# Performance work log

Hardware: AMD Instinct MI355X
Metric: run time of the kernel (lower is better)

The kernel has to match this reference:

```python
import jax, jax.numpy as jnp
import numpy as np

B, S, D_MODEL, D_K, D_V = 4, 2048, 512, 64, 64
TEMPERATURE = 8.0  # sqrt(d_k)


def setup_inputs() -> dict:
    key = jax.random.key(0)
    ks = jax.random.split(key, 12)
    q = jax.random.normal(ks[0], (B, S, D_MODEL), jnp.float32)
    k = jax.random.normal(ks[1], (B, S, D_MODEL), jnp.float32)
    v = jax.random.normal(ks[2], (B, S, D_MODEL), jnp.float32)
    g_bias = jax.random.normal(ks[3], (B, S, S), jnp.float32)
    mask = jax.random.bernoulli(ks[4], 0.25, (B, S, S))  # True = masked out
    sq = np.sqrt(2.0 / (D_MODEL + D_K)).astype(np.float32)
    sv = np.sqrt(2.0 / (D_MODEL + D_V)).astype(np.float32)
    Wq = jax.random.normal(ks[5], (D_MODEL, D_K), jnp.float32) * sq
    Wk = jax.random.normal(ks[6], (D_MODEL, D_K), jnp.float32) * sq
    Wv = jax.random.normal(ks[7], (D_MODEL, D_V), jnp.float32) * sv
    bq = jnp.zeros((D_K,), jnp.float32)
    bk = jnp.zeros((D_K,), jnp.float32)
    bv = jnp.zeros((D_V,), jnp.float32)
    lim = np.sqrt(6.0 / (D_V + D_MODEL)).astype(np.float32)  # xavier_uniform
    Wfc = jax.random.uniform(ks[8], (D_V, D_MODEL), jnp.float32, -lim, lim)
    bfc = jnp.zeros((D_MODEL,), jnp.float32)
    tau = jnp.float32(30.0)
    return {"q": q, "k": k, "v": v, "g_bias": g_bias, "mask": mask,
            "Wq": Wq, "bq": bq, "Wk": Wk, "bk": bk, "Wv": Wv, "bv": bv,
            "Wfc": Wfc, "bfc": bfc, "tau": tau}


def reference(q, k, v, g_bias, mask, Wq, bq, Wk, bk, Wv, bv, Wfc, bfc, tau):
    qp = q @ Wq + bq                                   # [B,S,dk]
    kp = k @ Wk + bk                                   # [B,S,dk]
    vp = v @ Wv + bv                                   # [B,S,dv]
    attn = jnp.einsum('bqd,bkd->bqk', qp, kp) / TEMPERATURE
    attn = attn + g_bias / (2.0 * tau ** 2)            # temperature-dependent Gaussian bias
    attn = jnp.where(mask, -jnp.inf, attn)
    p = jax.nn.softmax(attn, axis=2)                   # dropout = identity (eval mode)
    out = jnp.einsum('bqk,bkd->bqd', p, vp)            # [B,S,dv]
    return out @ Wfc + bfc                             # [B,S,d_model]
```

## Files before the change

### kernel.cpp

```cpp
#include <hip/hip_runtime.h>

#define NB 4
#define SS 2048
#define DM 512
#define DD 64
#define NR (NB*SS)
#define PH 128
#define NKS 8

typedef __attribute__((ext_vector_type(8))) short bf16x8;
typedef __attribute__((ext_vector_type(4))) float f32x4;

static __device__ __forceinline__ unsigned short f2b(float f) {
  union { float f; unsigned u; } x; x.f = f;
  unsigned r = x.u + 0x7FFFu + ((x.u >> 16) & 1u);
  return (unsigned short)(r >> 16);
}
static __device__ __forceinline__ float b2f(unsigned short h) {
  union { unsigned u; float f; } x; x.u = ((unsigned)h) << 16; return x.f;
}
static __device__ __forceinline__ bf16x8 ld8(const unsigned short* p) {
  union { uint4 u; bf16x8 v; } x; x.u = *(const uint4*)p; return x.v;
}
static __device__ __forceinline__ void glds16(const void* g, void* l) {
  auto gp = (const __attribute__((address_space(1))) unsigned*)((__UINTPTR_TYPE__)g);
  auto lp = (__attribute__((address_space(3))) unsigned*)((__UINTPTR_TYPE__)l);
  __builtin_amdgcn_global_load_lds(gp, lp, 16, 0, 0);
}

__global__ __launch_bounds__(256) void detect_mask(const unsigned* __restrict__ mw,
                                                   int nwords, int* __restrict__ part) {
  const int gid = blockIdx.x * 256 + threadIdx.x;
  const int nthr = gridDim.x * 256;
  int vi = 0, vf = 0, vu = 0;
  for (long i = (long)gid * 64; i < nwords; i += (long)nthr * 64) {
    unsigned w = mw[i];
    vi |= (w > 1u);
    vf |= ((w != 0u) & (w != 0x3F800000u));
    vu |= ((w & 0xFEFEFEFEu) != 0u);
  }
  __shared__ int sh[3];
  if (threadIdx.x < 3) sh[threadIdx.x] = 0;
  __syncthreads();
  int lane = threadIdx.x & 63;
  unsigned long long b;
  b = __ballot(vi); if (lane == 0 && b) sh[0] = 1;
  b = __ballot(vf); if (lane == 0 && b) sh[1] = 1;
  b = __ballot(vu); if (lane == 0 && b) sh[2] = 1;
  __syncthreads();
  if (threadIdx.x < 3) part[blockIdx.x * 4 + threadIdx.x] = sh[threadIdx.x];
}

__global__ __launch_bounds__(256) void prep(
    const float* __restrict__ Wq, const float* __restrict__ Wk, const float* __restrict__ Wv,
    unsigned short* __restrict__ Wt,
    const float* __restrict__ Wfc, unsigned short* __restrict__ WfcT) {
  const int bid = blockIdx.x;
  const int t = threadIdx.x;
  if (bid < 24) {
    const int p = bid >> 3;
    const float* W = (p == 0) ? Wq : ((p == 1) ? Wk : Wv);
    const int k0 = (bid & 7) * 64;
    const int n0 = (t & 15) * 4;
    #pragma unroll
    for (int p2 = 0; p2 < 4; ++p2) {
      int k = k0 + (t >> 4) + 16 * p2;
      float4 w = *(const float4*)(W + (size_t)k * DD + n0);
      Wt[(size_t)(p * DD + n0 + 0) * DM + k] = f2b(w.x);
      Wt[(size_t)(p * DD + n0 + 1) * DM + k] = f2b(w.y);
      Wt[(size_t)(p * DD + n0 + 2) * DM + k] = f2b(w.z);
      Wt[(size_t)(p * DD + n0 + 3) * DM + k] = f2b(w.w);
    }
  } else {
    const int n0 = (bid - 24) * 64;
    __shared__ unsigned short wt[64][68];
    {
      int k = t >> 2, j = (t & 3) * 16;
      #pragma unroll
      for (int u = 0; u < 4; ++u) {
        float4 w = *(const float4*)(Wfc + (size_t)k * DM + n0 + j + 4 * u);
        wt[k][j + 4 * u + 0] = f2b(w.x);
        wt[k][j + 4 * u + 1] = f2b(w.y);
        wt[k][j + 4 * u + 2] = f2b(w.z);
        wt[k][j + 4 * u + 3] = f2b(w.w);
      }
    }
    __syncthreads();
    {
      int n = t >> 2, kq = (t & 3) * 16;
      unsigned short tmp[16];
      #pragma unroll
      for (int u = 0; u < 16; ++u) tmp[u] = wt[kq + u][n];
      *(uint4*)(WfcT + (size_t)(n0 + n) * DD + kq) = *(uint4*)&tmp[0];
      *(uint4*)(WfcT + (size_t)(n0 + n) * DD + kq + 8) = *(uint4*)&tmp[8];
    }
  }
}

__global__ __launch_bounds__(256, 4) void proj_mfma(
    const float* __restrict__ q, const float* __restrict__ k, const float* __restrict__ v,
    const unsigned short* __restrict__ Wt,
    const float* __restrict__ bq, const float* __restrict__ bk, const float* __restrict__ bv,
    unsigned short* __restrict__ qp, unsigned short* __restrict__ kp,
    unsigned short* __restrict__ vpT) {
  const int p = blockIdx.y;
  const float* X = (p == 0) ? q : ((p == 1) ? k : v);
  const float* bias = (p == 0) ? bq : ((p == 1) ? bk : bv);
  unsigned short* out = (p == 0) ? qp : kp;
  const int row0 = blockIdx.x * 64;
  const int tid = threadIdx.x;
  const int wq = tid >> 6, lane = tid & 63, g = lane >> 4, c = lane & 15;
  __shared__ unsigned short x_s[64][72];
  f32x4 acc[4];
  #pragma unroll
  for (int s = 0; s < 4; ++s) acc[s] = (f32x4){0.f, 0.f, 0.f, 0.f};
  const unsigned short* wbase = Wt + (size_t)p * DD * DM;

  for (int k0 = 0; k0 < DM; k0 += 64) {
    __syncthreads();
    #pragma unroll
    for (int pp = 0; pp < 4; ++pp) {
      int f = tid + 256 * pp;
      int r = f >> 4, c4 = (f & 15) << 2;
      float4 xv = *(const float4*)(X + (size_t)(row0 + r) * DM + k0 + c4);
      uint2 u;
      u.x = (unsigned)f2b(xv.x) | ((unsigned)f2b(xv.y) << 16);
      u.y = (unsigned)f2b(xv.z) | ((unsigned)f2b(xv.w) << 16);
      *(uint2*)&x_s[r][c4] = u;
    }
    __syncthreads();
    const unsigned short* xrow = &x_s[wq * 16 + c][0];
    bf16x8 a0 = ld8(xrow + 8 * g);
    bf16x8 a1 = ld8(xrow + 32 + 8 * g);
    #pragma unroll
    for (int s = 0; s < 4; ++s) {
      const unsigned short* wrow = wbase + (size_t)(16 * s + c) * DM + k0;
      bf16x8 b0 = ld8(wrow + 8 * g);
      bf16x8 b1 = ld8(wrow + 32 + 8 * g);
      acc[s] = __builtin_amdgcn_mfma_f32_16x16x32_bf16(a0, b0, acc[s], 0, 0, 0);
      acc[s] = __builtin_amdgcn_mfma_f32_16x16x32_bf16(a1, b1, acc[s], 0, 0, 0);
    }
  }
  if (p != 2) {
    #pragma unroll
    for (int s = 0; s < 4; ++s) {
      float bs = bias[16 * s + c];
      #pragma unroll
      for (int r = 0; r < 4; ++r) {
        int row = row0 + wq * 16 + 4 * g + r;
        out[(size_t)row * DD + 16 * s + c] = f2b(acc[s][r] + bs);
      }
    }
  } else {
    __syncthreads();
    #pragma unroll
    for (int s = 0; s < 4; ++s) {
      float bs = bias[16 * s + c];
      #pragma unroll
      for (int r = 0; r < 4; ++r)
        x_s[16 * s + c][wq * 16 + 4 * g + r] = f2b(acc[s][r] + bs);
    }
    __syncthreads();
    int d = tid >> 2, q4 = (tid & 3) * 16;
    int bb = row0 >> 11, s0 = row0 & (SS - 1);
    unsigned short* dst = vpT + ((size_t)bb * DD + d) * SS + s0 + q4;
    *(uint4*)dst = *(uint4*)&x_s[d][q4];
    *(uint4*)(dst + 8) = *(uint4*)&x_s[d][q4 + 8];
  }
}

template<bool BYTE>
static __device__ __forceinline__ void attn_body(
    unsigned short* k_sf, unsigned short* v_tf, unsigned short* bias_s,
    unsigned short (*p_s)[16][72],
    const unsigned short* __restrict__ qp, const unsigned short* __restrict__ kp,
    const unsigned short* __restrict__ vpT, const float* __restrict__ g_bias,
    const void* __restrict__ mask, float bscale,
    int b, int qb, int wq, int g, int c, int lane, int kbeg,
    int ks, float* __restrict__ part_o, float* __restrict__ part_ml) {

  const int qw = qb * 64 + wq * 16;
  const unsigned short* qrow = qp + (size_t)(b * SS + qw + c) * DD;
  bf16x8 qf0 = ld8(qrow + 8 * g);
  bf16x8 qf1 = ld8(qrow + 32 + 8 * g);
  const unsigned short* kglob = kp + (size_t)b * SS * DD;
  const unsigned short* vglob = vpT + (size_t)b * DD * SS;

  float m_r = -1e30f, l_r = 0.f;
  f32x4 o[4];
  #pragma unroll
  for (int s = 0; s < 4; ++s) o[s] = (f32x4){0.f, 0.f, 0.f, 0.f};

  #pragma unroll 1
  for (int p = 0; p < 2; ++p) {
    const int kb = kbeg + p * PH;
    if (p) __syncthreads();

    {
      const int rl = wq * 16 + (lane >> 5);
      const int key4 = (lane & 31) * 4;
      #pragma unroll
      for (int u = 0; u < 8; ++u) {
        const int row_l = rl + u * 2;
        const size_t idx = (size_t)(b * SS + qb * 64 + row_l) * SS + kb + key4;
        f32x4 bv = *(const f32x4*)(g_bias + idx);
        unsigned short h[4];
        if (BYTE) {
          unsigned m = *(const unsigned*)((const unsigned char*)mask + idx);
          #pragma unroll
          for (int e = 0; e < 4; ++e)
            h[e] = ((m >> (8 * e)) & 0xFFu) ? (unsigned short)0xFF80u
                                            : f2b(bv[e] * bscale);
        } else {
          uint4 m = *(const uint4*)((const unsigned*)mask + idx);
          unsigned mw[4] = {m.x, m.y, m.z, m.w};
          #pragma unroll
          for (int e = 0; e < 4; ++e)
            h[e] = mw[e] ? (unsigned short)0xFF80u : f2b(bv[e] * bscale);
        }
        uint2 w;
        w.x = (unsigned)h[0] | ((unsigned)h[1] << 16);
        w.y = (unsigned)h[2] | ((unsigned)h[3] << 16);
        *(uint2*)&bias_s[row_l * 140 + key4] = w;
      }
    }
    #pragma unroll
    for (int u = 0; u < 4; ++u) {
      int iw = wq * 4 + u;
      {
        int row = iw * 8 + (lane >> 3);
        int sgr = (lane & 7) ^ (row & 7);
        glds16(kglob + (size_t)(kb + row) * DD + sgr * 8, k_sf + iw * 512);
      }
      {
        int row = iw * 4 + (lane >> 4);
        int sgr = (lane & 15) ^ (row & 7);
        glds16(vglob + (size_t)row * SS + kb + sgr * 8, v_tf + iw * 512);
      }
    }
    __syncthreads();

    #pragma unroll 1
    for (int kt = 0; kt < PH; kt += 64) {
      f32x4 sa[4];
      #pragma unroll
      for (int i = 0; i < 4; ++i) sa[i] = (f32x4){0.f, 0.f, 0.f, 0.f};
      #pragma unroll
      for (int i = 0; i < 4; ++i) {
        int r = kt + 16 * i + c;
        const unsigned short* krw = k_sf + r * 64;
        bf16x8 a0 = ld8(krw + ((g ^ (r & 7)) << 3));
        bf16x8 a1 = ld8(krw + (((4 + g) ^ (r & 7)) << 3));
        sa[i] = __builtin_amdgcn_mfma_f32_16x16x32_bf16(a0, qf0, sa[i], 0, 0, 0);
        sa[i] = __builtin_amdgcn_mfma_f32_16x16x32_bf16(a1, qf1, sa[i], 0, 0, 0);
      }
      float sc[16];
      const int brow = (wq * 16 + c) * 140;
      #pragma unroll
      for (int i = 0; i < 4; ++i) {
        uint2 bw = *(const uint2*)&bias_s[brow + kt + 16 * i + 4 * g];
        sc[4 * i + 0] = sa[i][0] * 0.125f + b2f((unsigned short)(bw.x & 0xFFFFu));
        sc[4 * i + 1] = sa[i][1] * 0.125f + b2f((unsigned short)(bw.x >> 16));
        sc[4 * i + 2] = sa[i][2] * 0.125f + b2f((unsigned short)(bw.y & 0xFFFFu));
        sc[4 * i + 3] = sa[i][3] * 0.125f + b2f((unsigned short)(bw.y >> 16));
      }
      float mx = sc[0];
      #pragma unroll
      for (int i2 = 1; i2 < 16; ++i2) mx = fmaxf(mx, sc[i2]);
      mx = fmaxf(mx, __shfl_xor(mx, 16));
      mx = fmaxf(mx, __shfl_xor(mx, 32));
      float mn = fmaxf(m_r, mx);
      float scl = __expf(m_r - mn);
      float sum = 0.f;
      #pragma unroll
      for (int i2 = 0; i2 < 16; ++i2) {
        sc[i2] = __expf(sc[i2] - mn);
        sum += sc[i2];
      }
      sum += __shfl_xor(sum, 16);
      sum += __shfl_xor(sum, 32);
      l_r = l_r * scl + sum;
      m_r = mn;
      #pragma unroll
      for (int i = 0; i < 4; ++i) {
        uint2 u;
        u.x = (unsigned)f2b(sc[4 * i]) | ((unsigned)f2b(sc[4 * i + 1]) << 16);
        u.y = (unsigned)f2b(sc[4 * i + 2]) | ((unsigned)f2b(sc[4 * i + 3]) << 16);
        *(uint2*)&p_s[wq][c][16 * i + 4 * g] = u;
      }
      float scl4[4];
      #pragma unroll
      for (int r = 0; r < 4; ++r) scl4[r] = __shfl(scl, 4 * g + r);
      #pragma unroll
      for (int s2 = 0; s2 < 4; ++s2) {
        #pragma unroll
        for (int r = 0; r < 4; ++r) o[s2][r] *= scl4[r];
      }
      bf16x8 pa0 = ld8(&p_s[wq][c][8 * g]);
      bf16x8 pa1 = ld8(&p_s[wq][c][32 + 8 * g]);
      const int gb0 = kt >> 3;
      #pragma unroll
      for (int s2 = 0; s2 < 4; ++s2) {
        int row = 16 * s2 + c;
        const unsigned short* vr = v_tf + row * PH;
        bf16x8 v0 = ld8(vr + (((gb0 + g) ^ (row & 7)) << 3));
        bf16x8 v1 = ld8(vr + (((gb0 + 4 + g) ^ (row & 7)) << 3));
        o[s2] = __builtin_amdgcn_mfma_f32_16x16x32_bf16(pa0, v0, o[s2], 0, 0, 0);
        o[s2] = __builtin_amdgcn_mfma_f32_16x16x32_bf16(pa1, v1, o[s2], 0, 0, 0);
      }
    }
  }
  const size_t gr0 = (size_t)b * SS + qw;
  #pragma unroll
  for (int s2 = 0; s2 < 4; ++s2) {
    #pragma unroll
    for (int r = 0; r < 4; ++r)
      part_o[((size_t)ks * NR + gr0 + 4 * g + r) * DD + 16 * s2 + c] = o[s2][r];
  }
  if (g == 0) {
    size_t row = (size_t)ks * NR + gr0 + c;
    part_ml[row * 2] = m_r;
    part_ml[row * 2 + 1] = l_r;
  }
}

__global__ __launch_bounds__(256, 2) void attn_mfma(
    const unsigned short* __restrict__ qp, const unsigned short* __restrict__ kp,
    const unsigned short* __restrict__ vpT, const float* __restrict__ g_bias,
    const void* __restrict__ mask, const int* __restrict__ part,
    const float* __restrict__ tau, float* __restrict__ part_o,
    float* __restrict__ part_ml) {
  __shared__ unsigned short k_sf[PH * 64];
  __shared__ unsigned short v_tf[64 * PH];
  __shared__ unsigned short bias_s[64 * 140];
  __shared__ unsigned short p_s[4][16][72];
  __shared__ int shf[3];
  const int tid = threadIdx.x;
  if (tid < 64) {
    int a0 = part[tid * 4], a1 = part[tid * 4 + 1], a2 = part[tid * 4 + 2];
    unsigned long long b0 = __ballot(a0 != 0);
    unsigned long long b1 = __ballot(a1 != 0);
    unsigned long long b2 = __ballot(a2 != 0);
    if (tid == 0) {
      shf[0] = b0 ? 1 : 0; shf[1] = b1 ? 1 : 0; shf[2] = b2 ? 1 : 0;
    }
  }
  __syncthreads();
  const bool bytemode = shf[0] && shf[1] && !shf[2];
  const int b = blockIdx.y;
  const int qb = blockIdx.x >> 3;
  const int ks = blockIdx.x & 7;
  const int wq = tid >> 6, lane = tid & 63, g = lane >> 4, c = lane & 15;
  const int kbeg = ks * (SS / NKS);
  const float tv = tau[0];
  const float bscale = 1.0f / (2.0f * tv * tv);
  if (bytemode)
    attn_body<true>(k_sf, v_tf, bias_s, p_s, qp, kp, vpT, g_bias, mask, bscale,
                    b, qb, wq, g, c, lane, kbeg, ks, part_o, part_ml);
  else
    attn_body<false>(k_sf, v_tf, bias_s, p_s, qp, kp, vpT, g_bias, mask, bscale,
                     b, qb, wq, g, c, lane, kbeg, ks, part_o, part_ml);
}

__global__ __launch_bounds__(256, 4) void fc_mfma(
    const float* __restrict__ part_o, const float* __restrict__ part_ml,
    const unsigned short* __restrict__ WfcT, const float* __restrict__ bfc,
    float* __restrict__ out, int nks) {
  const int row0 = blockIdx.x * 16;
  const int tid = threadIdx.x;
  const int w = tid >> 6, lane = tid & 63, g = lane >> 4, c = lane & 15;
  __shared__ unsigned short a16[16][72];
  {
    int r = tid >> 4, d4 = (tid & 15) * 4;
    size_t grow = (size_t)row0 + r;
    float M = -1e30f;
    for (int i = 0; i < nks; ++i) M = fmaxf(M, part_ml[((size_t)i * NR + grow) * 2]);
    float L = 0.f;
    float4 oa = {0.f, 0.f, 0.f, 0.f};
    for (int i = 0; i < nks; ++i) {
      float mi = part_ml[((size_t)i * NR + grow) * 2];
      float li = part_ml[((size_t)i * NR + grow) * 2 + 1];
      float wgt = __expf(mi - M);
      L += li * wgt;
      float4 ov = *(const float4*)&part_o[((size_t)i * NR + grow) * DD + d4];
      oa.x += wgt * ov.x; oa.y += wgt * ov.y; oa.z += wgt * ov.z; oa.w += wgt * ov.w;
    }
    float inv = (L > 0.f) ? 1.0f / L : 0.f;
    a16[r][d4 + 0] = f2b(oa.x * inv);
    a16[r][d4 + 1] = f2b(oa.y * inv);
    a16[r][d4 + 2] = f2b(oa.z * inv);
    a16[r][d4 + 3] = f2b(oa.w * inv);
  }
  __syncthreads();
  bf16x8 a0 = ld8(&a16[c][8 * g]);
  bf16x8 a1 = ld8(&a16[c][32 + 8 * g]);
  f32x4 acc[8];
  #pragma unroll
  for (int s = 0; s < 8; ++s) acc[s] = (f32x4){0.f, 0.f, 0.f, 0.f};
  #pragma unroll
  for (int s = 0; s < 8; ++s) {
    const unsigned short* bp = WfcT + (size_t)(128 * w + 16 * s + c) * DD;
    bf16x8 b0 = ld8(bp + 8 * g);
    bf16x8 b1 = ld8(bp + 32 + 8 * g);
    acc[s] = __builtin_amdgcn_mfma_f32_16x16x32_bf16(a0, b0, acc[s], 0, 0, 0);
    acc[s] = __builtin_amdgcn_mfma_f32_16x16x32_bf16(a1, b1, acc[s], 0, 0, 0);
  }
  #pragma unroll
  for (int s = 0; s < 8; ++s) {
    int col = 128 * w + 16 * s + c;
    float bb = bfc[col];
    #pragma unroll
    for (int rr = 0; rr < 4; ++rr)
      out[(size_t)(row0 + 4 * g + rr) * DM + col] = acc[s][rr] + bb;
  }
}

extern "C" void kernel_launch(void* const* d_in, const int* in_sizes, int n_in,
                              void* d_out, int out_size, void* d_ws, size_t ws_size,
                              hipStream_t stream) {
  const float* q    = (const float*)d_in[0];
  const float* k    = (const float*)d_in[1];
  const float* v    = (const float*)d_in[2];
  const float* gb   = (const float*)d_in[3];
  const void*  mask = d_in[4];
  const float* Wq   = (const float*)d_in[5];
  const float* bq   = (const float*)d_in[6];
  const float* Wk   = (const float*)d_in[7];
  const float* bk   = (const float*)d_in[8];
  const float* Wv   = (const float*)d_in[9];
  const float* bv   = (const float*)d_in[10];
  const float* Wfc  = (const float*)d_in[11];
  const float* bfc  = (const float*)d_in[12];
  const float* tau  = (const float*)d_in[13];
  float* out = (float*)d_out;

  char* ws = (char*)d_ws;
  int* part = (int*)(ws + 256);
  unsigned short* Wt   = (unsigned short*)(ws + 8192);
  unsigned short* WfcT = (unsigned short*)(ws + 8192 + 196608);
  unsigned short* qp  = (unsigned short*)(ws + 8192 + 196608 + 65536);
  unsigned short* kp  = qp + (size_t)NR * DD;
  unsigned short* vpT = kp + (size_t)NR * DD;
  float* part_o = (float*)(vpT + (size_t)NB * DD * SS);
  float* part_ml = part_o + (size_t)NKS * NR * DD;

  detect_mask<<<64, 256, 0, stream>>>((const unsigned*)mask, in_sizes[4] / 4, part);
  prep<<<32, 256, 0, stream>>>(Wq, Wk, Wv, Wt, Wfc, WfcT);
  proj_mfma<<<dim3(NR / 64, 3), 256, 0, stream>>>(q, k, v, Wt, bq, bk, bv, qp, kp, vpT);
  attn_mfma<<<dim3((SS / 64) * NKS, NB), 256, 0, stream>>>(
      qp, kp, vpT, gb, mask, part, tau, part_o, part_ml);
  fc_mfma<<<NR / 16, 256, 0, stream>>>(part_o, part_ml, WfcT, bfc, out, NKS);
}
```

Measured before the change: 78.93 us.

## Pre-pack masked scaled bias into swizzled bf16 tiles before attention

Adds a separate pack_bias kernel that folds the mask and tau scaling into bf16 bias values, written in a tiled, XOR-swizzled layout that matches the attention kernel's LDS layout. A new attn_packed kernel then loads bias tiles with direct global-to-LDS copies in 64-key phases, and runs at higher occupancy with smaller shared memory. The goal is to take the fp32 bias and mask decoding off the attention critical path. The cost is an extra full pass over g_bias and the mask plus a 32MB bf16 intermediate write and read. The path is used only when the workspace is large enough.

```diff
diff --git a/kernel.cpp b/kernel.cpp
--- a/kernel.cpp
+++ b/kernel.cpp
@@ -5,7 +5,6 @@
 #define DM 512
 #define DD 64
 #define NR (NB*SS)
-#define PH 128
 #define NKS 8
 
 typedef __attribute__((ext_vector_type(8))) short bf16x8;
@@ -49,6 +48,56 @@
   b = __ballot(vu); if (lane == 0 && b) sh[2] = 1;
   __syncthreads();
   if (threadIdx.x < 3) part[blockIdx.x * 4 + threadIdx.x] = sh[threadIdx.x];
+}
+
+__global__ __launch_bounds__(256) void pack_bias(
+    const float* __restrict__ g_bias, const void* __restrict__ mask,
+    const int* __restrict__ part, const float* __restrict__ tau,
+    unsigned short* __restrict__ biasP) {
+  __shared__ int shf[3];
+  const int tid = threadIdx.x;
+  if (tid < 64) {
+    int a0 = part[tid * 4], a1 = part[tid * 4 + 1], a2 = part[tid * 4 + 2];
+    unsigned long long b0 = __ballot(a0 != 0);
+    unsigned long long b1 = __ballot(a1 != 0);
+    unsigned long long b2 = __ballot(a2 != 0);
+    if (tid == 0) { shf[0] = b0 ? 1 : 0; shf[1] = b1 ? 1 : 0; shf[2] = b2 ? 1 : 0; }
+  }
+  __syncthreads();
+  const bool bytemode = shf[0] && shf[1] && !shf[2];
+  const float tv = tau[0];
+  const float bscale = 1.0f / (2.0f * tv * tv);
+  const size_t total = (size_t)NB * SS * (SS / 4);
+  const size_t stride = (size_t)gridDim.x * 256;
+  for (size_t u = (size_t)blockIdx.x * 256 + tid; u < total; u += stride) {
+    int b = (int)(u >> 20);
+    int rem = (int)(u & 0xFFFFFu);
+    int q = rem >> 9;
+    int k = (rem & 511) << 2;
+    size_t idx = (size_t)(b * SS + q) * SS + k;
+    f32x4 bv = *(const f32x4*)(g_bias + idx);
+    unsigned short h[4];
+    if (bytemode) {
+      unsigned m = *(const unsigned*)((const unsigned char*)mask + idx);
+      #pragma unroll
+      for (int e = 0; e < 4; ++e)
+        h[e] = ((m >> (8 * e)) & 0xFFu) ? (unsigned short)0xFF80u : f2b(bv[e] * bscale);
+    } else {
+      uint4 m = *(const uint4*)((const unsigned*)mask + idx);
+      unsigned mw[4] = {m.x, m.y, m.z, m.w};
+      #pragma unroll
+      for (int e = 0; e < 4; ++e)
+        h[e] = mw[e] ? (unsigned short)0xFF80u : f2b(bv[e] * bscale);
+    }
+    int ks = k >> 8, ph = (k >> 6) & 3, qb = q >> 6, row = q & 63;
+    int kgs = ((k >> 3) & 7) ^ (row & 7);
+    size_t dst = ((((((size_t)b * 8 + ks) * 32 + qb) * 4 + ph) * 64 + row) * 8 + kgs) * 8
+                 + (k & 7);
+    uint2 w;
+    w.x = (unsigned)h[0] | ((unsigned)h[1] << 16);
+    w.y = (unsigned)h[2] | ((unsigned)h[3] << 16);
+    *(uint2*)&biasP[dst] = w;
+  }
 }
 
 __global__ __launch_bounds__(256) void prep(
@@ -169,6 +218,130 @@
   }
 }
 
+__global__ __launch_bounds__(256, 4) void attn_packed(
+    const unsigned short* __restrict__ qp, const unsigned short* __restrict__ kp,
+    const unsigned short* __restrict__ vpT, const unsigned short* __restrict__ biasP,
+    float* __restrict__ part_o, float* __restrict__ part_ml) {
+  __shared__ unsigned short k_sf[64 * 64];
+  __shared__ unsigned short v_tf[64 * 64];
+  __shared__ unsigned short bias_s[64 * 64];
+  __shared__ unsigned short p_s[4][16][72];
+  const int b = blockIdx.y;
+  const int qb = blockIdx.x >> 3;
+  const int ks = blockIdx.x & 7;
+  const int tid = threadIdx.x;
+  const int wq = tid >> 6, lane = tid & 63, g = lane >> 4, c = lane & 15;
+  const int qw = qb * 64 + wq * 16;
+
+  const unsigned short* qrow = qp + (size_t)(b * SS + qw + c) * DD;
+  bf16x8 qf0 = ld8(qrow + 8 * g);
+  bf16x8 qf1 = ld8(qrow + 32 + 8 * g);
+  const unsigned short* kglob = kp + (size_t)b * SS * DD;
+  const unsigned short* vglob = vpT + (size_t)b * DD * SS;
+  const unsigned short* bblk = biasP + ((((size_t)b * 8 + ks) * 32 + qb) << 14);
+
+  float m_r = -1e30f, l_r = 0.f;
+  f32x4 o[4];
+  #pragma unroll
+  for (int s = 0; s < 4; ++s) o[s] = (f32x4){0.f, 0.f, 0.f, 0.f};
+
+  #pragma unroll 1
+  for (int p = 0; p < 4; ++p) {
+    const int kb = ks * 256 + p * 64;
+    if (p) __syncthreads();
+    const unsigned short* bsrc = bblk + (p << 12);
+    #pragma unroll
+    for (int u = 0; u < 2; ++u) {
+      int iw = wq * 2 + u;
+      int row = iw * 8 + (lane >> 3);
+      int sgr = (lane & 7) ^ (row & 7);
+      glds16(kglob + (size_t)(kb + row) * DD + sgr * 8, k_sf + iw * 512);
+      glds16(vglob + (size_t)row * SS + kb + sgr * 8, v_tf + iw * 512);
+      glds16(bsrc + iw * 512 + lane * 8, bias_s + iw * 512);
+    }
+    __syncthreads();
+
+    f32x4 sa[4];
+    #pragma unroll
+    for (int i = 0; i < 4; ++i) sa[i] = (f32x4){0.f, 0.f, 0.f, 0.f};
+    #pragma unroll
+    for (int i = 0; i < 4; ++i) {
+      int r = 16 * i + c;
+      const unsigned short* krw = k_sf + r * 64;
+      bf16x8 a0 = ld8(krw + ((g ^ (r & 7)) << 3));
+      bf16x8 a1 = ld8(krw + (((4 + g) ^ (r & 7)) << 3));
+      sa[i] = __builtin_amdgcn_mfma_f32_16x16x32_bf16(a0, qf0, sa[i], 0, 0, 0);
+      sa[i] = __builtin_amdgcn_mfma_f32_16x16x32_bf16(a1, qf1, sa[i], 0, 0, 0);
+    }
+    float sc[16];
+    const char* bb = (const char*)bias_s + (wq * 16 + c) * 128 + ((g & 1) ? 8 : 0);
+    #pragma unroll
+    for (int i = 0; i < 4; ++i) {
+      uint2 bw = *(const uint2*)(bb + (((2 * i + (g >> 1)) ^ (c & 7)) << 4));
+      sc[4 * i + 0] = sa[i][0] * 0.125f + b2f((unsigned short)(bw.x & 0xFFFFu));
+      sc[4 * i + 1] = sa[i][1] * 0.125f + b2f((unsigned short)(bw.x >> 16));
+      sc[4 * i + 2] = sa[i][2] * 0.125f + b2f((unsigned short)(bw.y & 0xFFFFu));
+      sc[4 * i + 3] = sa[i][3] * 0.125f + b2f((unsigned short)(bw.y >> 16));
+    }
+    float mx = sc[0];
+    #pragma unroll
+    for (int i2 = 1; i2 < 16; ++i2) mx = fmaxf(mx, sc[i2]);
+    mx = fmaxf(mx, __shfl_xor(mx, 16));
+    mx = fmaxf(mx, __shfl_xor(mx, 32));
+    float mn = fmaxf(m_r, mx);
+    float scl = __expf(m_r - mn);
+    float sum = 0.f;
+    #pragma unroll
+    for (int i2 = 0; i2 < 16; ++i2) {
+      sc[i2] = __expf(sc[i2] - mn);
+      sum += sc[i2];
+    }
+    sum += __shfl_xor(sum, 16);
+    sum += __shfl_xor(sum, 32);
+    l_r = l_r * scl + sum;
+    m_r = mn;
+    #pragma unroll
+    for (int i = 0; i < 4; ++i) {
+      uint2 u;
+      u.x = (unsigned)f2b(sc[4 * i]) | ((unsigned)f2b(sc[4 * i + 1]) << 16);
+      u.y = (unsigned)f2b(sc[4 * i + 2]) | ((unsigned)f2b(sc[4 * i + 3]) << 16);
+      *(uint2*)&p_s[wq][c][16 * i + 4 * g] = u;
+    }
+    float scl4[4];
+    #pragma unroll
+    for (int r = 0; r < 4; ++r) scl4[r] = __shfl(scl, 4 * g + r);
+    #pragma unroll
+    for (int s2 = 0; s2 < 4; ++s2) {
+      #pragma unroll
+      for (int r = 0; r < 4; ++r) o[s2][r] *= scl4[r];
+    }
+    bf16x8 pa0 = ld8(&p_s[wq][c][8 * g]);
+    bf16x8 pa1 = ld8(&p_s[wq][c][32 + 8 * g]);
+    #pragma unroll
+    for (int s2 = 0; s2 < 4; ++s2) {
+      int row = 16 * s2 + c;
+      const unsigned short* vr = v_tf + row * 64;
+      bf16x8 v0 = ld8(vr + ((g ^ (row & 7)) << 3));
+      bf16x8 v1 = ld8(vr + (((4 + g) ^ (row & 7)) << 3));
+      o[s2] = __builtin_amdgcn_mfma_f32_16x16x32_bf16(pa0, v0, o[s2], 0, 0, 0);
+      o[s2] = __builtin_amdgcn_mfma_f32_16x16x32_bf16(pa1, v1, o[s2], 0, 0, 0);
+    }
+  }
+  const size_t gr0 = (size_t)b * SS + qw;
+  #pragma unroll
+  for (int s2 = 0; s2 < 4; ++s2) {
+    #pragma unroll
+    for (int r = 0; r < 4; ++r)
+      part_o[((size_t)ks * NR + gr0 + 4 * g + r) * DD + 16 * s2 + c] = o[s2][r];
+  }
+  if (g == 0) {
+    size_t row = (size_t)ks * NR + gr0 + c;
+    part_ml[row * 2] = m_r;
+    part_ml[row * 2 + 1] = l_r;
+  }
+}
+
+#define PH 128
 template<bool BYTE>
 static __device__ __forceinline__ void attn_body(
     unsigned short* k_sf, unsigned short* v_tf, unsigned short* bias_s,
@@ -195,7 +368,6 @@
   for (int p = 0; p < 2; ++p) {
     const int kb = kbeg + p * PH;
     if (p) __syncthreads();
-
     {
       const int rl = wq * 16 + (lane >> 5);
       const int key4 = (lane & 31) * 4;
@@ -341,9 +513,7 @@
     unsigned long long b0 = __ballot(a0 != 0);
     unsigned long long b1 = __ballot(a1 != 0);
     unsigned long long b2 = __ballot(a2 != 0);
-    if (tid == 0) {
-      shf[0] = b0 ? 1 : 0; shf[1] = b1 ? 1 : 0; shf[2] = b2 ? 1 : 0;
-    }
+    if (tid == 0) { shf[0] = b0 ? 1 : 0; shf[1] = b1 ? 1 : 0; shf[2] = b2 ? 1 : 0; }
   }
   __syncthreads();
   const bool bytemode = shf[0] && shf[1] && !shf[2];
@@ -443,11 +613,21 @@
   unsigned short* vpT = kp + (size_t)NR * DD;
   float* part_o = (float*)(vpT + (size_t)NB * DD * SS);
   float* part_ml = part_o + (size_t)NKS * NR * DD;
+  unsigned short* biasP = (unsigned short*)(part_ml + (size_t)NKS * NR * 2);
+  size_t biasP_elems = (size_t)NB * 8 * 32 * 4 * 64 * 64;
+  size_t need = (size_t)((char*)(biasP + biasP_elems) - ws);
+  const bool use_pack = (ws_size >= need);
 
   detect_mask<<<64, 256, 0, stream>>>((const unsigned*)mask, in_sizes[4] / 4, part);
   prep<<<32, 256, 0, stream>>>(Wq, Wk, Wv, Wt, Wfc, WfcT);
   proj_mfma<<<dim3(NR / 64, 3), 256, 0, stream>>>(q, k, v, Wt, bq, bk, bv, qp, kp, vpT);
-  attn_mfma<<<dim3((SS / 64) * NKS, NB), 256, 0, stream>>>(
-      qp, kp, vpT, gb, mask, part, tau, part_o, part_ml);
+  if (use_pack) {
+    pack_bias<<<2048, 256, 0, stream>>>(gb, mask, part, tau, biasP);
+    attn_packed<<<dim3((SS / 64) * NKS, NB), 256, 0, stream>>>(
+        qp, kp, vpT, biasP, part_o, part_ml);
+  } else {
+    attn_mfma<<<dim3((SS / 64) * NKS, NB), 256, 0, stream>>>(
+        qp, kp, vpT, gb, mask, part, tau, part_o, part_ml);
+  }
   fc_mfma<<<NR / 16, 256, 0, stream>>>(part_o, part_ml, WfcT, bfc, out, NKS);
 }
```

Result: slower. 88.33 us (+11.9%).

## Stream raw fp32 bias and byte mask into LDS via direct global-to-LDS loads

Applied to the files above, without the earlier changes.

The attention kernel no longer converts g_bias and mask to a bf16 bias tile with per-thread register loads. It now copies the fp32 bias rows, and the byte mask in byte mode, into swizzled LDS with global_load_lds, then applies scale and masking while forming the scores. The key phase shrinks from two 128-key phases to four 64-key phases, and launch bounds rise to 3 blocks per CU. This aims to cut VALU conversion work and register pressure and to make bias loads asynchronous, at the cost of more barriers and more LDS per key.

```diff
diff --git a/kernel.cpp b/kernel.cpp
--- a/kernel.cpp
+++ b/kernel.cpp
@@ -5,7 +5,6 @@
 #define DM 512
 #define DD 64
 #define NR (NB*SS)
-#define PH 128
 #define NKS 8
 
 typedef __attribute__((ext_vector_type(8))) short bf16x8;
@@ -15,9 +14,6 @@
   union { float f; unsigned u; } x; x.f = f;
   unsigned r = x.u + 0x7FFFu + ((x.u >> 16) & 1u);
   return (unsigned short)(r >> 16);
-}
-static __device__ __forceinline__ float b2f(unsigned short h) {
-  union { unsigned u; float f; } x; x.u = ((unsigned)h) << 16; return x.f;
 }
 static __device__ __forceinline__ bf16x8 ld8(const unsigned short* p) {
   union { uint4 u; bf16x8 v; } x; x.u = *(const uint4*)p; return x.v;
@@ -171,13 +167,13 @@
 
 template<bool BYTE>
 static __device__ __forceinline__ void attn_body(
-    unsigned short* k_sf, unsigned short* v_tf, unsigned short* bias_s,
-    unsigned short (*p_s)[16][72],
+    unsigned short* k_sf, unsigned short* v_tf, float* bias_f,
+    unsigned char* mask_sb, unsigned short (*p_s)[16][72],
     const unsigned short* __restrict__ qp, const unsigned short* __restrict__ kp,
     const unsigned short* __restrict__ vpT, const float* __restrict__ g_bias,
     const void* __restrict__ mask, float bscale,
-    int b, int qb, int wq, int g, int c, int lane, int kbeg,
-    int ks, float* __restrict__ part_o, float* __restrict__ part_ml) {
+    int b, int qb, int wq, int g, int c, int lane, int ks,
+    float* __restrict__ part_o, float* __restrict__ part_ml) {
 
   const int qw = qb * 64 + wq * 16;
   const unsigned short* qrow = qp + (size_t)(b * SS + qw + c) * DD;
@@ -185,6 +181,9 @@
   bf16x8 qf1 = ld8(qrow + 32 + 8 * g);
   const unsigned short* kglob = kp + (size_t)b * SS * DD;
   const unsigned short* vglob = vpT + (size_t)b * DD * SS;
+  const float* gbb = g_bias + (size_t)(b * SS + qb * 64) * SS;
+  const unsigned char* mbb = (const unsigned char*)mask + (size_t)(b * SS + qb * 64) * SS;
+  const unsigned* mwb = (const unsigned*)mask + (size_t)(b * SS + qb * 64) * SS;
 
   float m_r = -1e30f, l_r = 0.f;
   f32x4 o[4];
@@ -192,122 +191,108 @@
   for (int s = 0; s < 4; ++s) o[s] = (f32x4){0.f, 0.f, 0.f, 0.f};
 
   #pragma unroll 1
-  for (int p = 0; p < 2; ++p) {
-    const int kb = kbeg + p * PH;
+  for (int p = 0; p < 4; ++p) {
+    const int kb = ks * 256 + p * 64;
     if (p) __syncthreads();
 
-    {
-      const int rl = wq * 16 + (lane >> 5);
-      const int key4 = (lane & 31) * 4;
+    #pragma unroll
+    for (int j = 0; j < 4; ++j) {
+      int u = wq * 4 + j;
+      int row = u * 4 + (lane >> 4);
+      int sgr = (lane & 15) ^ (row & 15);
+      glds16(gbb + (size_t)row * SS + kb + sgr * 4, (char*)bias_f + u * 1024);
+    }
+    #pragma unroll
+    for (int u = 0; u < 2; ++u) {
+      int iw = wq * 2 + u;
+      int row = iw * 8 + (lane >> 3);
+      int sgr = (lane & 7) ^ (row & 7);
+      glds16(kglob + (size_t)(kb + row) * DD + sgr * 8, k_sf + iw * 512);
+      glds16(vglob + (size_t)row * SS + kb + sgr * 8, v_tf + iw * 512);
+    }
+    if (BYTE) {
+      int row = wq * 16 + (lane >> 2);
+      int sgr = (lane & 3) ^ (row & 3);
+      glds16(mbb + (size_t)row * SS + kb + sgr * 16, mask_sb + wq * 1024);
+    }
+    __syncthreads();
+
+    f32x4 sa[4];
+    #pragma unroll
+    for (int i = 0; i < 4; ++i) sa[i] = (f32x4){0.f, 0.f, 0.f, 0.f};
+    #pragma unroll
+    for (int i = 0; i < 4; ++i) {
+      int r = 16 * i + c;
+      const unsigned short* krw = k_sf + r * 64;
+      bf16x8 a0 = ld8(krw + ((g ^ (r & 7)) << 3));
+      bf16x8 a1 = ld8(krw + (((4 + g) ^ (r & 7)) << 3));
+      sa[i] = __builtin_amdgcn_mfma_f32_16x16x32_bf16(a0, qf0, sa[i], 0, 0, 0);
+      sa[i] = __builtin_amdgcn_mfma_f32_16x16x32_bf16(a1, qf1, sa[i], 0, 0, 0);
+    }
+    float sc[16];
+    const int row = wq * 16 + c;
+    #pragma unroll
+    for (int i = 0; i < 4; ++i) {
+      f32x4 bv = *(const f32x4*)&bias_f[row * 64 + (((4 * i + g) ^ c) << 2)];
+      if (BYTE) {
+        unsigned mm = *(const unsigned*)&mask_sb[row * 64 + ((i ^ (c & 3)) << 4) + 4 * g];
+        #pragma unroll
+        for (int e = 0; e < 4; ++e) {
+          float x = sa[i][e] * 0.125f + bv[e] * bscale;
+          sc[4 * i + e] = ((mm >> (8 * e)) & 0xFFu) ? -1e30f : x;
+        }
+      } else {
+        uint4 mw4 = *(const uint4*)(mwb + (size_t)row * SS + kb + 16 * i + 4 * g);
+        unsigned mw[4] = {mw4.x, mw4.y, mw4.z, mw4.w};
+        #pragma unroll
+        for (int e = 0; e < 4; ++e) {
+          float x = sa[i][e] * 0.125f + bv[e] * bscale;
+          sc[4 * i + e] = mw[e] ? -1e30f : x;
+        }
+      }
+    }
+    float mx = sc[0];
+    #pragma unroll
+    for (int i2 = 1; i2 < 16; ++i2) mx = fmaxf(mx, sc[i2]);
+    mx = fmaxf(mx, __shfl_xor(mx, 16));
+    mx = fmaxf(mx, __shfl_xor(mx, 32));
+    float mn = fmaxf(m_r, mx);
+    float scl = __expf(m_r - mn);
+    float sum = 0.f;
+    #pragma unroll
+    for (int i2 = 0; i2 < 16; ++i2) {
+      sc[i2] = __expf(sc[i2] - mn);
+      sum += sc[i2];
+    }
+    sum += __shfl_xor(sum, 16);
+    sum += __shfl_xor(sum, 32);
+    l_r = l_r * scl + sum;
+    m_r = mn;
+    #pragma unroll
+    for (int i = 0; i < 4; ++i) {
+      uint2 u;
+      u.x = (unsigned)f2b(sc[4 * i]) | ((unsigned)f2b(sc[4 * i + 1]) << 16);
+      u.y = (unsigned)f2b(sc[4 * i + 2]) | ((unsigned)f2b(sc[4 * i + 3]) << 16);
+      *(uint2*)&p_s[wq][c][16 * i + 4 * g] = u;
+    }
+    float scl4[4];
+    #pragma unroll
+    for (int r = 0; r < 4; ++r) scl4[r] = __shfl(scl, 4 * g + r);
+    #pragma unroll
+    for (int s2 = 0; s2 < 4; ++s2) {
       #pragma unroll
-      for (int u = 0; u < 8; ++u) {
-        const int row_l = rl + u * 2;
-        const size_t idx = (size_t)(b * SS + qb * 64 + row_l) * SS + kb + key4;
-        f32x4 bv = *(const f32x4*)(g_bias + idx);
-        unsigned short h[4];
-        if (BYTE) {
-          unsigned m = *(const unsigned*)((const unsigned char*)mask + idx);
-          #pragma unroll
-          for (int e = 0; e < 4; ++e)
-            h[e] = ((m >> (8 * e)) & 0xFFu) ? (unsigned short)0xFF80u
-                                            : f2b(bv[e] * bscale);
-        } else {
-          uint4 m = *(const uint4*)((const unsigned*)mask + idx);
-          unsigned mw[4] = {m.x, m.y, m.z, m.w};
-          #pragma unroll
-          for (int e = 0; e < 4; ++e)
-            h[e] = mw[e] ? (unsigned short)0xFF80u : f2b(bv[e] * bscale);
-        }
-        uint2 w;
-        w.x = (unsigned)h[0] | ((unsigned)h[1] << 16);
-        w.y = (unsigned)h[2] | ((unsigned)h[3] << 16);
-        *(uint2*)&bias_s[row_l * 140 + key4] = w;
-      }
-    }
-    #pragma unroll
-    for (int u = 0; u < 4; ++u) {
-      int iw = wq * 4 + u;
-      {
-        int row = iw * 8 + (lane >> 3);
-        int sgr = (lane & 7) ^ (row & 7);
-        glds16(kglob + (size_t)(kb + row) * DD + sgr * 8, k_sf + iw * 512);
-      }
-      {
-        int row = iw * 4 + (lane >> 4);
-        int sgr = (lane & 15) ^ (row & 7);
-        glds16(vglob + (size_t)row * SS + kb + sgr * 8, v_tf + iw * 512);
-      }
-    }
-    __syncthreads();
-
-    #pragma unroll 1
-    for (int kt = 0; kt < PH; kt += 64) {
-      f32x4 sa[4];
-      #pragma unroll
-      for (int i = 0; i < 4; ++i) sa[i] = (f32x4){0.f, 0.f, 0.f, 0.f};
-      #pragma unroll
-      for (int i = 0; i < 4; ++i) {
-        int r = kt + 16 * i + c;
-        const unsigned short* krw = k_sf + r * 64;
-        bf16x8 a0 = ld8(krw + ((g ^ (r & 7)) << 3));
-        bf16x8 a1 = ld8(krw + (((4 + g) ^ (r & 7)) << 3));
-        sa[i] = __builtin_amdgcn_mfma_f32_16x16x32_bf16(a0, qf0, sa[i], 0, 0, 0);
-        sa[i] = __builtin_amdgcn_mfma_f32_16x16x32_bf16(a1, qf1, sa[i], 0, 0, 0);
-      }
-      float sc[16];
-      const int brow = (wq * 16 + c) * 140;
-      #pragma unroll
-      for (int i = 0; i < 4; ++i) {
-        uint2 bw = *(const uint2*)&bias_s[brow + kt + 16 * i + 4 * g];
-        sc[4 * i + 0] = sa[i][0] * 0.125f + b2f((unsigned short)(bw.x & 0xFFFFu));
-        sc[4 * i + 1] = sa[i][1] * 0.125f + b2f((unsigned short)(bw.x >> 16));
-        sc[4 * i + 2] = sa[i][2] * 0.125f + b2f((unsigned short)(bw.y & 0xFFFFu));
-        sc[4 * i + 3] = sa[i][3] * 0.125f + b2f((unsigned short)(bw.y >> 16));
-      }
-      float mx = sc[0];
-      #pragma unroll
-      for (int i2 = 1; i2 < 16; ++i2) mx = fmaxf(mx, sc[i2]);
-      mx = fmaxf(mx, __shfl_xor(mx, 16));
-      mx = fmaxf(mx, __shfl_xor(mx, 32));
-      float mn = fmaxf(m_r, mx);
-      float scl = __expf(m_r - mn);
-      float sum = 0.f;
-      #pragma unroll
-      for (int i2 = 0; i2 < 16; ++i2) {
-        sc[i2] = __expf(sc[i2] - mn);
-        sum += sc[i2];
-      }
-      sum += __shfl_xor(sum, 16);
-      sum += __shfl_xor(sum, 32);
-      l_r = l_r * scl + sum;
-      m_r = mn;
-      #pragma unroll
-      for (int i = 0; i < 4; ++i) {
-        uint2 u;
-        u.x = (unsigned)f2b(sc[4 * i]) | ((unsigned)f2b(sc[4 * i + 1]) << 16);
-        u.y = (unsigned)f2b(sc[4 * i + 2]) | ((unsigned)f2b(sc[4 * i + 3]) << 16);
-        *(uint2*)&p_s[wq][c][16 * i + 4 * g] = u;
-      }
-      float scl4[4];
-      #pragma unroll
-      for (int r = 0; r < 4; ++r) scl4[r] = __shfl(scl, 4 * g + r);
-      #pragma unroll
-      for (int s2 = 0; s2 < 4; ++s2) {
-        #pragma unroll
-        for (int r = 0; r < 4; ++r) o[s2][r] *= scl4[r];
-      }
-      bf16x8 pa0 = ld8(&p_s[wq][c][8 * g]);
-      bf16x8 pa1 = ld8(&p_s[wq][c][32 + 8 * g]);
-      const int gb0 = kt >> 3;
-      #pragma unroll
-      for (int s2 = 0; s2 < 4; ++s2) {
-        int row = 16 * s2 + c;
-        const unsigned short* vr = v_tf + row * PH;
-        bf16x8 v0 = ld8(vr + (((gb0 + g) ^ (row & 7)) << 3));
-        bf16x8 v1 = ld8(vr + (((gb0 + 4 + g) ^ (row & 7)) << 3));
-        o[s2] = __builtin_amdgcn_mfma_f32_16x16x32_bf16(pa0, v0, o[s2], 0, 0, 0);
-        o[s2] = __builtin_amdgcn_mfma_f32_16x16x32_bf16(pa1, v1, o[s2], 0, 0, 0);
-      }
+      for (int r = 0; r < 4; ++r) o[s2][r] *= scl4[r];
+    }
+    bf16x8 pa0 = ld8(&p_s[wq][c][8 * g]);
+    bf16x8 pa1 = ld8(&p_s[wq][c][32 + 8 * g]);
+    #pragma unroll
+    for (int s2 = 0; s2 < 4; ++s2) {
+      int row2 = 16 * s2 + c;
+      const unsigned short* vr = v_tf + row2 * 64;
+      bf16x8 v0 = ld8(vr + ((g ^ (row2 & 7)) << 3));
+      bf16x8 v1 = ld8(vr + (((4 + g) ^ (row2 & 7)) << 3));
+      o[s2] = __builtin_amdgcn_mfma_f32_16x16x32_bf16(pa0, v0, o[s2], 0, 0, 0);
+      o[s2] = __builtin_amdgcn_mfma_f32_16x16x32_bf16(pa1, v1, o[s2], 0, 0, 0);
     }
   }
   const size_t gr0 = (size_t)b * SS + qw;
@@ -324,15 +309,16 @@
   }
 }
 
-__global__ __launch_bounds__(256, 2) void attn_mfma(
+__global__ __launch_bounds__(256, 3) void attn_raw(
     const unsigned short* __restrict__ qp, const unsigned short* __restrict__ kp,
     const unsigned short* __restrict__ vpT, const float* __restrict__ g_bias,
     const void* __restrict__ mask, const int* __restrict__ part,
     const float* __restrict__ tau, float* __restrict__ part_o,
     float* __restrict__ part_ml) {
-  __shared__ unsigned short k_sf[PH * 64];
-  __shared__ unsigned short v_tf[64 * PH];
-  __shared__ unsigned short bias_s[64 * 140];
+  __shared__ unsigned short k_sf[64 * 64];
+  __shared__ unsigned short v_tf[64 * 64];
+  __shared__ float bias_f[64 * 64];
+  __shared__ unsigned char mask_sb[64 * 64];
   __shared__ unsigned short p_s[4][16][72];
   __shared__ int shf[3];
   const int tid = threadIdx.x;
@@ -341,9 +327,7 @@
     unsigned long long b0 = __ballot(a0 != 0);
     unsigned long long b1 = __ballot(a1 != 0);
     unsigned long long b2 = __ballot(a2 != 0);
-    if (tid == 0) {
-      shf[0] = b0 ? 1 : 0; shf[1] = b1 ? 1 : 0; shf[2] = b2 ? 1 : 0;
-    }
+    if (tid == 0) { shf[0] = b0 ? 1 : 0; shf[1] = b1 ? 1 : 0; shf[2] = b2 ? 1 : 0; }
   }
   __syncthreads();
   const bool bytemode = shf[0] && shf[1] && !shf[2];
@@ -351,15 +335,14 @@
   const int qb = blockIdx.x >> 3;
   const int ks = blockIdx.x & 7;
   const int wq = tid >> 6, lane = tid & 63, g = lane >> 4, c = lane & 15;
-  const int kbeg = ks * (SS / NKS);
   const float tv = tau[0];
   const float bscale = 1.0f / (2.0f * tv * tv);
   if (bytemode)
-    attn_body<true>(k_sf, v_tf, bias_s, p_s, qp, kp, vpT, g_bias, mask, bscale,
-                    b, qb, wq, g, c, lane, kbeg, ks, part_o, part_ml);
+    attn_body<true>(k_sf, v_tf, bias_f, mask_sb, p_s, qp, kp, vpT, g_bias, mask,
+                    bscale, b, qb, wq, g, c, lane, ks, part_o, part_ml);
   else
-    attn_body<false>(k_sf, v_tf, bias_s, p_s, qp, kp, vpT, g_bias, mask, bscale,
-                     b, qb, wq, g, c, lane, kbeg, ks, part_o, part_ml);
+    attn_body<false>(k_sf, v_tf, bias_f, mask_sb, p_s, qp, kp, vpT, g_bias, mask,
+                     bscale, b, qb, wq, g, c, lane, ks, part_o, part_ml);
 }
 
 __global__ __launch_bounds__(256, 4) void fc_mfma(
@@ -447,7 +430,7 @@
   detect_mask<<<64, 256, 0, stream>>>((const unsigned*)mask, in_sizes[4] / 4, part);
   prep<<<32, 256, 0, stream>>>(Wq, Wk, Wv, Wt, Wfc, WfcT);
   proj_mfma<<<dim3(NR / 64, 3), 256, 0, stream>>>(q, k, v, Wt, bq, bk, bv, qp, kp, vpT);
-  attn_mfma<<<dim3((SS / 64) * NKS, NB), 256, 0, stream>>>(
+  attn_raw<<<dim3((SS / 64) * NKS, NB), 256, 0, stream>>>(
       qp, kp, vpT, gb, mask, part, tau, part_o, part_ml);
   fc_mfma<<<NR / 16, 256, 0, stream>>>(part_o, part_ml, WfcT, bfc, out, NKS);
 }
```

New measurement: 74.23 us. 1.06x faster.
